# Optimization experiments

Measured on AMD Instinct MI355X. Metric: run time of the kernel, lower is better.

The kernel has to match this reference:

```python
import jax, jax.numpy as jnp
import numpy as np

N, D = 8192, 256
ALPHA, BETA, K = 50.0, 1.0, 2


def setup_inputs() -> dict:
    key = jax.random.key(0)
    k1, k2, k3, k4 = jax.random.split(key, 4)
    Q = jax.random.normal(k1, (N, D), dtype=jnp.float32)
    # 0/1 similarity structure; diagonal forced nonzero so no row is fully masked
    sim = jax.random.randint(k2, (N, N), 0, 2).astype(jnp.float32)
    sim = sim.at[jnp.arange(N), jnp.arange(N)].set(1.0)
    # nn.Linear(in_dim, in_dim) params: y = x @ W.T + b
    bound = 1.0 / np.sqrt(D)
    W = jax.random.uniform(k3, (D, D), jnp.float32, -bound, bound)
    b = jax.random.uniform(k4, (D,), jnp.float32, -bound, bound)
    return {"Q": Q, "sim_mat": sim, "W": W, "b": b}


def reference(Q, sim_mat, W, b):
    mask = sim_mat == 0  # (N, N) bool, constant across iterations
    H = Q
    for _ in range(K):
        H_proj = H @ W.T + b                      # (N, d)
        scores = H_proj @ H_proj.T                # (N, N)
        scores = jnp.where(mask, -jnp.inf, scores)
        lamb = jax.nn.softmax(scores, axis=1)     # (N, N)
        numerator = ALPHA * Q + BETA * (lamb @ H)
        denominator = ALPHA + BETA * jnp.sum(lamb, axis=1, keepdims=True)
        H = numerator / denominator
    return H
```

## Files before the change

### kernel.cpp

```cpp
#include <hip/hip_runtime.h>
#include <hip/hip_bf16.h>

#define NN 8192
#define DD 256
#define ALPHA 50.0f
#define BETA 1.0f
#define THR 10.0f
#define KQ 8
#define KEYS (NN / KQ)
#define STEPS (KEYS / 32)
#define QROWS 128

typedef __attribute__((ext_vector_type(8))) short short8;
typedef __attribute__((ext_vector_type(4))) float f32x4;

static __device__ __forceinline__ ushort f2bf(float f) {
    union { __hip_bfloat16 h; ushort u; } v;
    v.h = __float2bfloat16(f);
    return v.u;
}
static __device__ __forceinline__ float bf2f(ushort u) {
    union { unsigned u; float f; } v; v.u = ((unsigned)u) << 16;
    return v.f;
}
static __device__ __forceinline__ void gl_lds16(const void* g, void* l) {
    __builtin_amdgcn_global_load_lds(
        (const __attribute__((address_space(1))) unsigned int*)g,
        (__attribute__((address_space(3))) unsigned int*)l, 16, 0, 0);
}

__global__ void k_wconv(const float* __restrict__ W, ushort* __restrict__ Wb) {
    int i = blockIdx.x * 256 + threadIdx.x;
    Wb[i] = f2bf(W[i]);
}

__global__ __launch_bounds__(256) void k_pack(const float* __restrict__ sim,
                                              unsigned* __restrict__ bits) {
    __shared__ unsigned char nibs[256];
    int row = blockIdx.x;
    int tid = threadIdx.x;
    for (int p = 0; p < 8; ++p) {
        int col = p * 1024 + tid * 4;
        float4 v = *reinterpret_cast<const float4*>(sim + (size_t)row * NN + col);
        unsigned char nib = (unsigned char)((v.x != 0.f) | ((v.y != 0.f) << 1) |
                                            ((v.z != 0.f) << 2) | ((v.w != 0.f) << 3));
        nibs[tid] = nib;
        __syncthreads();
        if (tid < 32) {
            unsigned word = 0;
#pragma unroll
            for (int i = 0; i < 8; ++i) word |= ((unsigned)nibs[tid * 8 + i]) << (4 * i);
            bits[row * (NN / 32) + p * 32 + tid] = word;
        }
        __syncthreads();
    }
}

__global__ __launch_bounds__(256) void k_convert(const float* __restrict__ H,
                                                 ushort* __restrict__ Hv,
                                                 ushort* __restrict__ Hvt) {
    __shared__ ushort T[64][72];
    int tile = blockIdx.x;
    int r0 = (tile >> 2) * 64;
    int c0 = (tile & 3) * 64;
    int tid = threadIdx.x;
    int tr = tid >> 4;
    int tc = (tid & 15) * 4;
    for (int i = 0; i < 4; ++i) {
        int r = tr + i * 16;
        float4 v = *reinterpret_cast<const float4*>(H + (size_t)(r0 + r) * DD + c0 + tc);
        ushort4 o;
        o.x = f2bf(v.x); o.y = f2bf(v.y); o.z = f2bf(v.z); o.w = f2bf(v.w);
        *reinterpret_cast<ushort4*>(Hv + (size_t)(r0 + r) * DD + c0 + tc) = o;
        T[tc + 0][r] = o.x; T[tc + 1][r] = o.y; T[tc + 2][r] = o.z; T[tc + 3][r] = o.w;
    }
    __syncthreads();
    for (int i = 0; i < 4; ++i) {
        int c = tr + i * 16;
        ushort4 o;
        o.x = T[c][tc + 0]; o.y = T[c][tc + 1]; o.z = T[c][tc + 2]; o.w = T[c][tc + 3];
        *reinterpret_cast<ushort4*>(Hvt + (size_t)(c0 + c) * NN + r0 + tc) = o;
    }
}

__global__ __launch_bounds__(256) void k_proj(const ushort* __restrict__ Hv,
                                              const ushort* __restrict__ Wb,
                                              const float* __restrict__ b,
                                              ushort* __restrict__ Hp) {
    int w = threadIdx.x >> 6;
    int lane = threadIdx.x & 63;
    int row0 = (blockIdx.x >> 1) * 64 + w * 16;
    int ch = blockIdx.x & 1;
    int lr = lane & 15;
    int lk = lane >> 4;
    short8 af[8];
    for (int kk = 0; kk < 8; ++kk)
        af[kk] = *reinterpret_cast<const short8*>(Hv + (size_t)(row0 + lr) * DD + kk * 32 + lk * 8);
    for (int t = 0; t < 8; ++t) {
        f32x4 acc = {0.f, 0.f, 0.f, 0.f};
        int col = (ch * 8 + t) * 16 + lr;
        for (int kk = 0; kk < 8; ++kk) {
            short8 bf = *reinterpret_cast<const short8*>(Wb + (size_t)col * DD + kk * 32 + lk * 8);
            acc = __builtin_amdgcn_mfma_f32_16x16x32_bf16(af[kk], bf, acc, 0, 0, 0);
        }
        float bias = b[col];
        for (int j = 0; j < 4; ++j) {
            int row = row0 + lk * 4 + j;
            Hp[(size_t)row * DD + col] = f2bf(acc[j] + bias);
        }
    }
}

#define PSTR 40
#define KBYTES (32 * 256 * 2)
#define VBYTES (256 * 32 * 2)
#define PBYTES (8 * 16 * PSTR * 2)
#define BBYTES (QROWS * 32 * 4)
#define SMEM_ATTN (3 * KBYTES + 3 * VBYTES + PBYTES + BBYTES)
__global__ __launch_bounds__(512) void k_attn(const ushort* __restrict__ Hp,
                                              const ushort* __restrict__ Hvt,
                                              const unsigned* __restrict__ bits,
                                              ushort* __restrict__ Opart,
                                              float* __restrict__ mpart,
                                              float* __restrict__ lpart) {
    extern __shared__ char smem[];
    ushort* KlB = (ushort*)smem;
    ushort* VlB = (ushort*)(smem + 3 * KBYTES);
    ushort* Pl  = (ushort*)(smem + 3 * KBYTES + 3 * VBYTES);
    unsigned* Bl = (unsigned*)(smem + 3 * KBYTES + 3 * VBYTES + PBYTES);

    const int tid = threadIdx.x;
    const int w = tid >> 6;
    const int lane = tid & 63;
    const int lr = lane & 15;
    const int lk = lane >> 4;
    const int bid = blockIdx.x;
    const int kq = bid & 7;
    const int qt = bid >> 3;
    const int rw0 = qt * QROWS + w * 16;
    const int kstart = kq * KEYS;

    int kSrc[2], vSrc[2], dstO[2];
#pragma unroll
    for (int i = 0; i < 2; ++i) {
        int S = i * 512 + tid;
        int rK = S >> 5, cpK = S & 31;
        kSrc[i] = rK * 256 + (cpK ^ (rK & 7)) * 8;
        int rV = S >> 2, cpV = S & 3;
        vSrc[i] = rV * NN + (cpV ^ ((rV >> 2) & 3)) * 8;
        dstO[i] = S * 8;
    }
    auto stageK = [&](int buf, int kb) {
        const ushort* Kg = Hp + (size_t)kb * DD;
        ushort* base = KlB + buf * (32 * 256);
#pragma unroll
        for (int i = 0; i < 2; ++i) gl_lds16(Kg + kSrc[i], base + dstO[i]);
    };
    auto stageV = [&](int buf, int kb) {
        const ushort* Vg = Hvt + kb;
        ushort* base = VlB + buf * (256 * 32);
#pragma unroll
        for (int i = 0; i < 2; ++i) gl_lds16(Vg + vSrc[i], base + dstO[i]);
    };

    int Koff[8];
#pragma unroll
    for (int kk = 0; kk < 8; ++kk)
        Koff[kk] = (lr << 9) + ((((kk << 2) + lk) ^ (lr & 7)) << 4);
    const int vBase = (lr << 6) + ((lk ^ ((lr >> 2) & 3)) << 4);

    short8 qf[8];
#pragma unroll
    for (int kk = 0; kk < 8; ++kk)
        qf[kk] = *reinterpret_cast<const short8*>(Hp + (size_t)(rw0 + lr) * DD + kk * 32 + lk * 8);

    f32x4 o[17];
#pragma unroll
    for (int t = 0; t < 17; ++t) o[t] = {0.f, 0.f, 0.f, 0.f};
    float m[4] = {-1e30f, -1e30f, -1e30f, -1e30f};

    short8 ones;
#pragma unroll
    for (int e = 0; e < 8; ++e) ones[e] = (short)0x3f80;

    {
        const unsigned* Bg = bits + (size_t)(qt * QROWS) * (NN / 32) + kq * 32;
#pragma unroll
        for (int i = 0; i < 2; ++i) {
            int S = i * 512 + tid;
            int r = S >> 3, c = S & 7;
            gl_lds16(Bg + (size_t)r * (NN / 32) + c * 4, Bl + S * 4);
        }
    }
    stageK(0, kstart);
    stageV(0, kstart);
    stageK(1, kstart + 32);
    stageV(1, kstart + 32);
    asm volatile("s_waitcnt vmcnt(4)" ::: "memory");
    __builtin_amdgcn_s_barrier();
    __builtin_amdgcn_sched_barrier(0);

    ushort* Pw = Pl + (size_t)w * 16 * PSTR;
    const int mrow = (w * 16 + lk * 4) * 32;
    int cur = 0;
    for (int step = 0; step < STEPS; ++step) {
        const int kb = kstart + step * 32;
        const bool staged = (step + 2 < STEPS);
        if (staged) {
            int nb = cur + 2; if (nb >= 3) nb -= 3;
            stageK(nb, kb + 64);
            stageV(nb, kb + 64);
        }
        unsigned mwj[4];
#pragma unroll
        for (int j = 0; j < 4; ++j) mwj[j] = Bl[mrow + j * 32 + step];

        const char* Kb = (const char*)(KlB + cur * (32 * 256));
        f32x4 s0 = {0.f, 0.f, 0.f, 0.f}, s1 = {0.f, 0.f, 0.f, 0.f};
        __builtin_amdgcn_s_setprio(1);
#pragma unroll
        for (int kk = 0; kk < 8; ++kk) {
            short8 k0 = *reinterpret_cast<const short8*>(Kb + Koff[kk]);
            short8 k1 = *reinterpret_cast<const short8*>(Kb + Koff[kk] + (16 << 9));
            s0 = __builtin_amdgcn_mfma_f32_16x16x32_bf16(qf[kk], k0, s0, 0, 0, 0);
            s1 = __builtin_amdgcn_mfma_f32_16x16x32_bf16(qf[kk], k1, s1, 0, 0, 0);
        }
        __builtin_amdgcn_s_setprio(0);
        float c = -1e30f;
#pragma unroll
        for (int j = 0; j < 4; ++j) {
            float a0 = ((mwj[j] >> lr) & 1u) ? s0[j] : -1e30f;
            float a1 = ((mwj[j] >> (lr + 16)) & 1u) ? s1[j] : -1e30f;
            s0[j] = a0; s1[j] = a1;
            c = fmaxf(c, fmaxf(a0, a1) - m[j]);
        }
        if (__any(c > THR)) {
#pragma unroll
            for (int j = 0; j < 4; ++j) {
                float mx = fmaxf(s0[j], s1[j]);
                mx = fmaxf(mx, __shfl_xor(mx, 1));
                mx = fmaxf(mx, __shfl_xor(mx, 2));
                mx = fmaxf(mx, __shfl_xor(mx, 4));
                mx = fmaxf(mx, __shfl_xor(mx, 8));
                float mn = fmaxf(m[j], mx);
                float scale = __expf(m[j] - mn);
                m[j] = mn;
#pragma unroll
                for (int t = 0; t < 17; ++t) o[t][j] *= scale;
            }
        }
#pragma unroll
        for (int j = 0; j < 4; ++j) {
            Pw[(lk * 4 + j) * PSTR + lr]      = f2bf(__expf(s0[j] - m[j]));
            Pw[(lk * 4 + j) * PSTR + 16 + lr] = f2bf(__expf(s1[j] - m[j]));
        }
        asm volatile("s_waitcnt lgkmcnt(0)" ::: "memory");
        __builtin_amdgcn_sched_barrier(0);
        short8 pa = *reinterpret_cast<const short8*>(Pw + lr * PSTR + lk * 8);
        const char* Vb = (const char*)(VlB + cur * (256 * 32));
        __builtin_amdgcn_s_setprio(1);
#pragma unroll
        for (int t = 0; t < 16; ++t) {
            short8 vf = *reinterpret_cast<const short8*>(Vb + vBase + (t << 10));
            o[t] = __builtin_amdgcn_mfma_f32_16x16x32_bf16(pa, vf, o[t], 0, 0, 0);
        }
        o[16] = __builtin_amdgcn_mfma_f32_16x16x32_bf16(pa, ones, o[16], 0, 0, 0);
        __builtin_amdgcn_s_setprio(0);
        if (staged) asm volatile("s_waitcnt vmcnt(4)" ::: "memory");
        else        asm volatile("s_waitcnt vmcnt(0)" ::: "memory");
        __builtin_amdgcn_s_barrier();
        __builtin_amdgcn_sched_barrier(0);
        cur = (cur == 2) ? 0 : cur + 1;
    }

    ushort* op = Opart + ((size_t)kq * NN + rw0) * DD;
#pragma unroll
    for (int t = 0; t < 16; ++t)
#pragma unroll
        for (int j = 0; j < 4; ++j)
            op[(size_t)(lk * 4 + j) * DD + t * 16 + lr] = f2bf(o[t][j]);
    if (lr == 0) {
#pragma unroll
        for (int j = 0; j < 4; ++j) {
            mpart[kq * NN + rw0 + lk * 4 + j] = m[j];
            lpart[kq * NN + rw0 + lk * 4 + j] = o[16][j];
        }
    }
}

__global__ __launch_bounds__(256) void k_merge8(const ushort* __restrict__ Opart,
                                                const float* __restrict__ mpart,
                                                const float* __restrict__ lpart,
                                                const float* __restrict__ Qo,
                                                float* __restrict__ dst) {
    int w = threadIdx.x >> 6;
    int lane = threadIdx.x & 63;
    int r0 = blockIdx.x * 32 + w * 8;
    for (int rr = 0; rr < 8; ++rr) {
        int r = r0 + rr;
        float mv[8], f[8];
        float M = -1e30f;
#pragma unroll
        for (int p = 0; p < 8; ++p) { mv[p] = mpart[p * NN + r]; M = fmaxf(M, mv[p]); }
        float L = 0.f;
#pragma unroll
        for (int p = 0; p < 8; ++p) { f[p] = __expf(mv[p] - M); L += f[p] * lpart[p * NN + r]; }
        float invL = 1.0f / L;
        int c = lane * 4;
        float a0 = 0.f, a1 = 0.f, a2 = 0.f, a3 = 0.f;
#pragma unroll
        for (int p = 0; p < 8; ++p) {
            ushort4 u = *reinterpret_cast<const ushort4*>(Opart + ((size_t)p * NN + r) * DD + c);
            a0 += f[p] * bf2f(u.x); a1 += f[p] * bf2f(u.y);
            a2 += f[p] * bf2f(u.z); a3 += f[p] * bf2f(u.w);
        }
        float4 qv = *reinterpret_cast<const float4*>(Qo + (size_t)r * DD + c);
        float4 ov;
        ov.x = (ALPHA * qv.x + a0 * invL) * (1.0f / (ALPHA + BETA));
        ov.y = (ALPHA * qv.y + a1 * invL) * (1.0f / (ALPHA + BETA));
        ov.z = (ALPHA * qv.z + a2 * invL) * (1.0f / (ALPHA + BETA));
        ov.w = (ALPHA * qv.w + a3 * invL) * (1.0f / (ALPHA + BETA));
        *reinterpret_cast<float4*>(dst + (size_t)r * DD + c) = ov;
    }
}

extern "C" void kernel_launch(void* const* d_in, const int* in_sizes, int n_in,
                              void* d_out, int out_size, void* d_ws, size_t ws_size,
                              hipStream_t stream) {
    const float* Q   = (const float*)d_in[0];
    const float* sim = (const float*)d_in[1];
    const float* W   = (const float*)d_in[2];
    const float* b   = (const float*)d_in[3];
    float* out = (float*)d_out;

    char* ws = (char*)d_ws;
    size_t off = 0;
    ushort* Hv   = (ushort*)(ws + off); off += (size_t)NN * DD * 2;
    ushort* HvtA = (ushort*)(ws + off); off += (size_t)NN * DD * 2;
    ushort* HvtB = (ushort*)(ws + off); off += (size_t)NN * DD * 2;
    ushort* Hp   = (ushort*)(ws + off); off += (size_t)NN * DD * 2;
    ushort* Wb   = (ushort*)(ws + off); off += (size_t)DD * DD * 2;
    unsigned* bits = (unsigned*)(ws + off); off += (size_t)NN * (NN / 32) * 4;
    float*  H1   = (float*)(ws + off);  off += (size_t)NN * DD * 4;
    ushort* Opart = (ushort*)(ws + off); off += (size_t)KQ * NN * DD * 2;
    float*  mpart = (float*)(ws + off);  off += (size_t)KQ * NN * 4;
    float*  lpart = (float*)(ws + off);  off += (size_t)KQ * NN * 4;

    (void)hipFuncSetAttribute((const void*)k_attn,
                              hipFuncAttributeMaxDynamicSharedMemorySize, SMEM_ATTN);

    k_wconv<<<DD * DD / 256, 256, 0, stream>>>(W, Wb);
    k_pack<<<NN, 256, 0, stream>>>(sim, bits);
    k_convert<<<(NN / 64) * (DD / 64), 256, 0, stream>>>(Q, Hv, HvtA);

    k_proj<<<NN / 32, 256, 0, stream>>>(Hv, Wb, b, Hp);
    k_attn<<<(NN / QROWS) * KQ, 512, SMEM_ATTN, stream>>>(Hp, HvtA, bits, Opart, mpart, lpart);
    k_merge8<<<NN / 32, 256, 0, stream>>>(Opart, mpart, lpart, Q, H1);
    k_convert<<<(NN / 64) * (DD / 64), 256, 0, stream>>>(H1, Hv, HvtB);

    k_proj<<<NN / 32, 256, 0, stream>>>(Hv, Wb, b, Hp);
    k_attn<<<(NN / QROWS) * KQ, 512, SMEM_ATTN, stream>>>(Hp, HvtB, bits, Opart, mpart, lpart);
    k_merge8<<<NN / 32, 256, 0, stream>>>(Opart, mpart, lpart, Q, out);
}
```

Measured before the change: 351.5 us.

## Load K fragments directly into registers instead of staging through LDS

Removes the triple-buffered K tile in shared memory. Each wave now prefetches its own K MFMA fragments from global memory into registers one step ahead, with vmcnt waits adjusted to match. This cuts LDS footprint and LDS reads for the QK^T product. The cost is redundant global loads across the 8 waves and 64 more vector registers per lane, which risks spills or lower occupancy.

```diff
diff --git a/kernel.cpp b/kernel.cpp
--- a/kernel.cpp
+++ b/kernel.cpp
@@ -112,11 +112,10 @@
 }
 
 #define PSTR 40
-#define KBYTES (32 * 256 * 2)
 #define VBYTES (256 * 32 * 2)
 #define PBYTES (8 * 16 * PSTR * 2)
 #define BBYTES (QROWS * 32 * 4)
-#define SMEM_ATTN (3 * KBYTES + 3 * VBYTES + PBYTES + BBYTES)
+#define SMEM_ATTN (3 * VBYTES + PBYTES + BBYTES)
 __global__ __launch_bounds__(512) void k_attn(const ushort* __restrict__ Hp,
                                               const ushort* __restrict__ Hvt,
                                               const unsigned* __restrict__ bits,
@@ -124,10 +123,9 @@
                                               float* __restrict__ mpart,
                                               float* __restrict__ lpart) {
     extern __shared__ char smem[];
-    ushort* KlB = (ushort*)smem;
-    ushort* VlB = (ushort*)(smem + 3 * KBYTES);
-    ushort* Pl  = (ushort*)(smem + 3 * KBYTES + 3 * VBYTES);
-    unsigned* Bl = (unsigned*)(smem + 3 * KBYTES + 3 * VBYTES + PBYTES);
+    ushort* VlB = (ushort*)smem;
+    ushort* Pl  = (ushort*)(smem + 3 * VBYTES);
+    unsigned* Bl = (unsigned*)(smem + 3 * VBYTES + PBYTES);
 
     const int tid = threadIdx.x;
     const int w = tid >> 6;
@@ -140,22 +138,14 @@
     const int rw0 = qt * QROWS + w * 16;
     const int kstart = kq * KEYS;
 
-    int kSrc[2], vSrc[2], dstO[2];
+    int vSrc[2], dstO[2];
 #pragma unroll
     for (int i = 0; i < 2; ++i) {
         int S = i * 512 + tid;
-        int rK = S >> 5, cpK = S & 31;
-        kSrc[i] = rK * 256 + (cpK ^ (rK & 7)) * 8;
         int rV = S >> 2, cpV = S & 3;
         vSrc[i] = rV * NN + (cpV ^ ((rV >> 2) & 3)) * 8;
         dstO[i] = S * 8;
     }
-    auto stageK = [&](int buf, int kb) {
-        const ushort* Kg = Hp + (size_t)kb * DD;
-        ushort* base = KlB + buf * (32 * 256);
-#pragma unroll
-        for (int i = 0; i < 2; ++i) gl_lds16(Kg + kSrc[i], base + dstO[i]);
-    };
     auto stageV = [&](int buf, int kb) {
         const ushort* Vg = Hvt + kb;
         ushort* base = VlB + buf * (256 * 32);
@@ -163,10 +153,6 @@
         for (int i = 0; i < 2; ++i) gl_lds16(Vg + vSrc[i], base + dstO[i]);
     };
 
-    int Koff[8];
-#pragma unroll
-    for (int kk = 0; kk < 8; ++kk)
-        Koff[kk] = (lr << 9) + ((((kk << 2) + lk) ^ (lr & 7)) << 4);
     const int vBase = (lr << 6) + ((lk ^ ((lr >> 2) & 3)) << 4);
 
     short8 qf[8];
@@ -192,11 +178,19 @@
             gl_lds16(Bg + (size_t)r * (NN / 32) + c * 4, Bl + S * 4);
         }
     }
-    stageK(0, kstart);
     stageV(0, kstart);
-    stageK(1, kstart + 32);
     stageV(1, kstart + 32);
-    asm volatile("s_waitcnt vmcnt(4)" ::: "memory");
+    short8 kreg[16];
+    {
+        const ushort* kp0 = Hp + (size_t)(kstart + lr) * DD + lk * 8;
+        const ushort* kp1 = kp0 + (size_t)16 * DD;
+#pragma unroll
+        for (int kk = 0; kk < 8; ++kk) {
+            kreg[kk]     = *reinterpret_cast<const short8*>(kp0 + kk * 32);
+            kreg[8 + kk] = *reinterpret_cast<const short8*>(kp1 + kk * 32);
+        }
+    }
+    asm volatile("s_waitcnt vmcnt(18)" ::: "memory");
     __builtin_amdgcn_s_barrier();
     __builtin_amdgcn_sched_barrier(0);
 
@@ -205,27 +199,31 @@
     int cur = 0;
     for (int step = 0; step < STEPS; ++step) {
         const int kb = kstart + step * 32;
-        const bool staged = (step + 2 < STEPS);
-        if (staged) {
+        if (step + 2 < STEPS) {
             int nb = cur + 2; if (nb >= 3) nb -= 3;
-            stageK(nb, kb + 64);
             stageV(nb, kb + 64);
         }
         unsigned mwj[4];
 #pragma unroll
         for (int j = 0; j < 4; ++j) mwj[j] = Bl[mrow + j * 32 + step];
 
-        const char* Kb = (const char*)(KlB + cur * (32 * 256));
         f32x4 s0 = {0.f, 0.f, 0.f, 0.f}, s1 = {0.f, 0.f, 0.f, 0.f};
         __builtin_amdgcn_s_setprio(1);
 #pragma unroll
         for (int kk = 0; kk < 8; ++kk) {
-            short8 k0 = *reinterpret_cast<const short8*>(Kb + Koff[kk]);
-            short8 k1 = *reinterpret_cast<const short8*>(Kb + Koff[kk] + (16 << 9));
-            s0 = __builtin_amdgcn_mfma_f32_16x16x32_bf16(qf[kk], k0, s0, 0, 0, 0);
-            s1 = __builtin_amdgcn_mfma_f32_16x16x32_bf16(qf[kk], k1, s1, 0, 0, 0);
+            s0 = __builtin_amdgcn_mfma_f32_16x16x32_bf16(qf[kk], kreg[kk], s0, 0, 0, 0);
+            s1 = __builtin_amdgcn_mfma_f32_16x16x32_bf16(qf[kk], kreg[8 + kk], s1, 0, 0, 0);
         }
         __builtin_amdgcn_s_setprio(0);
+        if (step + 1 < STEPS) {
+            const ushort* kp0 = Hp + (size_t)(kb + 32 + lr) * DD + lk * 8;
+            const ushort* kp1 = kp0 + (size_t)16 * DD;
+#pragma unroll
+            for (int kk = 0; kk < 8; ++kk) {
+                kreg[kk]     = *reinterpret_cast<const short8*>(kp0 + kk * 32);
+                kreg[8 + kk] = *reinterpret_cast<const short8*>(kp1 + kk * 32);
+            }
+        }
         float c = -1e30f;
 #pragma unroll
         for (int j = 0; j < 4; ++j) {
@@ -266,10 +264,15 @@
         }
         o[16] = __builtin_amdgcn_mfma_f32_16x16x32_bf16(pa, ones, o[16], 0, 0, 0);
         __builtin_amdgcn_s_setprio(0);
-        if (staged) asm volatile("s_waitcnt vmcnt(4)" ::: "memory");
-        else        asm volatile("s_waitcnt vmcnt(0)" ::: "memory");
-        __builtin_amdgcn_s_barrier();
-        __builtin_amdgcn_sched_barrier(0);
+        if (step + 2 < STEPS) {
+            asm volatile("s_waitcnt vmcnt(18)" ::: "memory");
+            __builtin_amdgcn_s_barrier();
+            __builtin_amdgcn_sched_barrier(0);
+        } else if (step + 1 < STEPS) {
+            asm volatile("s_waitcnt vmcnt(16)" ::: "memory");
+            __builtin_amdgcn_s_barrier();
+            __builtin_amdgcn_sched_barrier(0);
+        }
         cur = (cur == 2) ? 0 : cur + 1;
     }
 
```

After: 616.6 us. +75.5%, slower.

## Use 64-key tiles with double buffering and one barrier per tile in attention

Applied to the files above, without the earlier changes.

The attention kernel now processes 64 keys per iteration instead of 32. It moves from a triple-buffered 32-key pipeline to a double-buffered 64-key pipeline, which halves the number of block barriers and keeps LDS use about the same. The V tile layout and its swizzle change to match the 64-key width. The QK MFMAs for both 32-key halves are issued together before the two softmax and PV halves run. The cost is a shallower prefetch (one tile ahead with a full vmcnt(0) wait) and higher register pressure from four score accumulators.

```diff
diff --git a/kernel.cpp b/kernel.cpp
--- a/kernel.cpp
+++ b/kernel.cpp
@@ -8,7 +8,8 @@
 #define THR 10.0f
 #define KQ 8
 #define KEYS (NN / KQ)
-#define STEPS (KEYS / 32)
+#define KTILE 64
+#define ITERS (KEYS / KTILE)
 #define QROWS 128
 
 typedef __attribute__((ext_vector_type(8))) short short8;
@@ -112,11 +113,11 @@
 }
 
 #define PSTR 40
-#define KBYTES (32 * 256 * 2)
-#define VBYTES (256 * 32 * 2)
+#define KBYTES (KTILE * 256 * 2)
+#define VBYTES (256 * KTILE * 2)
 #define PBYTES (8 * 16 * PSTR * 2)
 #define BBYTES (QROWS * 32 * 4)
-#define SMEM_ATTN (3 * KBYTES + 3 * VBYTES + PBYTES + BBYTES)
+#define SMEM_ATTN (2 * KBYTES + 2 * VBYTES + PBYTES + BBYTES)
 __global__ __launch_bounds__(512) void k_attn(const ushort* __restrict__ Hp,
                                               const ushort* __restrict__ Hvt,
                                               const unsigned* __restrict__ bits,
@@ -125,9 +126,9 @@
                                               float* __restrict__ lpart) {
     extern __shared__ char smem[];
     ushort* KlB = (ushort*)smem;
-    ushort* VlB = (ushort*)(smem + 3 * KBYTES);
-    ushort* Pl  = (ushort*)(smem + 3 * KBYTES + 3 * VBYTES);
-    unsigned* Bl = (unsigned*)(smem + 3 * KBYTES + 3 * VBYTES + PBYTES);
+    ushort* VlB = (ushort*)(smem + 2 * KBYTES);
+    ushort* Pl  = (ushort*)(smem + 2 * KBYTES + 2 * VBYTES);
+    unsigned* Bl = (unsigned*)(smem + 2 * KBYTES + 2 * VBYTES + PBYTES);
 
     const int tid = threadIdx.x;
     const int w = tid >> 6;
@@ -140,34 +141,35 @@
     const int rw0 = qt * QROWS + w * 16;
     const int kstart = kq * KEYS;
 
-    int kSrc[2], vSrc[2], dstO[2];
-#pragma unroll
-    for (int i = 0; i < 2; ++i) {
+    int kSrc[4], vSrc[4], dstO[4];
+#pragma unroll
+    for (int i = 0; i < 4; ++i) {
         int S = i * 512 + tid;
         int rK = S >> 5, cpK = S & 31;
         kSrc[i] = rK * 256 + (cpK ^ (rK & 7)) * 8;
-        int rV = S >> 2, cpV = S & 3;
-        vSrc[i] = rV * NN + (cpV ^ ((rV >> 2) & 3)) * 8;
+        int rV = S >> 3, cpV = S & 7;
+        vSrc[i] = rV * NN + (cpV ^ (rV & 7)) * 8;
         dstO[i] = S * 8;
     }
     auto stageK = [&](int buf, int kb) {
         const ushort* Kg = Hp + (size_t)kb * DD;
-        ushort* base = KlB + buf * (32 * 256);
-#pragma unroll
-        for (int i = 0; i < 2; ++i) gl_lds16(Kg + kSrc[i], base + dstO[i]);
+        ushort* base = KlB + buf * (KTILE * 256);
+#pragma unroll
+        for (int i = 0; i < 4; ++i) gl_lds16(Kg + kSrc[i], base + dstO[i]);
     };
     auto stageV = [&](int buf, int kb) {
         const ushort* Vg = Hvt + kb;
-        ushort* base = VlB + buf * (256 * 32);
-#pragma unroll
-        for (int i = 0; i < 2; ++i) gl_lds16(Vg + vSrc[i], base + dstO[i]);
+        ushort* base = VlB + buf * (256 * KTILE);
+#pragma unroll
+        for (int i = 0; i < 4; ++i) gl_lds16(Vg + vSrc[i], base + dstO[i]);
     };
 
     int Koff[8];
 #pragma unroll
     for (int kk = 0; kk < 8; ++kk)
         Koff[kk] = (lr << 9) + ((((kk << 2) + lk) ^ (lr & 7)) << 4);
-    const int vBase = (lr << 6) + ((lk ^ ((lr >> 2) & 3)) << 4);
+    const int vBaseA = (lr << 7) + ((lk ^ (lr & 7)) << 4);
+    const int vBaseB = (lr << 7) + (((4 + lk) ^ (lr & 7)) << 4);
 
     short8 qf[8];
 #pragma unroll
@@ -194,83 +196,133 @@
     }
     stageK(0, kstart);
     stageV(0, kstart);
-    stageK(1, kstart + 32);
-    stageV(1, kstart + 32);
-    asm volatile("s_waitcnt vmcnt(4)" ::: "memory");
+    asm volatile("s_waitcnt vmcnt(0)" ::: "memory");
     __builtin_amdgcn_s_barrier();
     __builtin_amdgcn_sched_barrier(0);
 
     ushort* Pw = Pl + (size_t)w * 16 * PSTR;
     const int mrow = (w * 16 + lk * 4) * 32;
     int cur = 0;
-    for (int step = 0; step < STEPS; ++step) {
-        const int kb = kstart + step * 32;
-        const bool staged = (step + 2 < STEPS);
+    for (int it = 0; it < ITERS; ++it) {
+        const int kb = kstart + it * KTILE;
+        const bool staged = (it + 1 < ITERS);
         if (staged) {
-            int nb = cur + 2; if (nb >= 3) nb -= 3;
-            stageK(nb, kb + 64);
-            stageV(nb, kb + 64);
-        }
-        unsigned mwj[4];
-#pragma unroll
-        for (int j = 0; j < 4; ++j) mwj[j] = Bl[mrow + j * 32 + step];
-
-        const char* Kb = (const char*)(KlB + cur * (32 * 256));
-        f32x4 s0 = {0.f, 0.f, 0.f, 0.f}, s1 = {0.f, 0.f, 0.f, 0.f};
+            stageK(cur ^ 1, kb + KTILE);
+            stageV(cur ^ 1, kb + KTILE);
+        }
+        unsigned mwa[4], mwb[4];
+#pragma unroll
+        for (int j = 0; j < 4; ++j) {
+            mwa[j] = Bl[mrow + j * 32 + it * 2];
+            mwb[j] = Bl[mrow + j * 32 + it * 2 + 1];
+        }
+
+        const char* Kb = (const char*)(KlB + cur * (KTILE * 256));
+        f32x4 s0a = {0.f,0.f,0.f,0.f}, s1a = {0.f,0.f,0.f,0.f};
+        f32x4 s0b = {0.f,0.f,0.f,0.f}, s1b = {0.f,0.f,0.f,0.f};
         __builtin_amdgcn_s_setprio(1);
 #pragma unroll
         for (int kk = 0; kk < 8; ++kk) {
-            short8 k0 = *reinterpret_cast<const short8*>(Kb + Koff[kk]);
-            short8 k1 = *reinterpret_cast<const short8*>(Kb + Koff[kk] + (16 << 9));
-            s0 = __builtin_amdgcn_mfma_f32_16x16x32_bf16(qf[kk], k0, s0, 0, 0, 0);
-            s1 = __builtin_amdgcn_mfma_f32_16x16x32_bf16(qf[kk], k1, s1, 0, 0, 0);
+            short8 k0a = *reinterpret_cast<const short8*>(Kb + Koff[kk]);
+            short8 k1a = *reinterpret_cast<const short8*>(Kb + Koff[kk] + (16 << 9));
+            short8 k0b = *reinterpret_cast<const short8*>(Kb + Koff[kk] + (32 << 9));
+            short8 k1b = *reinterpret_cast<const short8*>(Kb + Koff[kk] + (48 << 9));
+            s0a = __builtin_amdgcn_mfma_f32_16x16x32_bf16(qf[kk], k0a, s0a, 0, 0, 0);
+            s1a = __builtin_amdgcn_mfma_f32_16x16x32_bf16(qf[kk], k1a, s1a, 0, 0, 0);
+            s0b = __builtin_amdgcn_mfma_f32_16x16x32_bf16(qf[kk], k0b, s0b, 0, 0, 0);
+            s1b = __builtin_amdgcn_mfma_f32_16x16x32_bf16(qf[kk], k1b, s1b, 0, 0, 0);
         }
         __builtin_amdgcn_s_setprio(0);
-        float c = -1e30f;
-#pragma unroll
-        for (int j = 0; j < 4; ++j) {
-            float a0 = ((mwj[j] >> lr) & 1u) ? s0[j] : -1e30f;
-            float a1 = ((mwj[j] >> (lr + 16)) & 1u) ? s1[j] : -1e30f;
-            s0[j] = a0; s1[j] = a1;
-            c = fmaxf(c, fmaxf(a0, a1) - m[j]);
-        }
-        if (__any(c > THR)) {
+
+        const char* Vb = (const char*)(VlB + cur * (256 * KTILE));
+        {
+            float c = -1e30f;
 #pragma unroll
             for (int j = 0; j < 4; ++j) {
-                float mx = fmaxf(s0[j], s1[j]);
-                mx = fmaxf(mx, __shfl_xor(mx, 1));
-                mx = fmaxf(mx, __shfl_xor(mx, 2));
-                mx = fmaxf(mx, __shfl_xor(mx, 4));
-                mx = fmaxf(mx, __shfl_xor(mx, 8));
-                float mn = fmaxf(m[j], mx);
-                float scale = __expf(m[j] - mn);
-                m[j] = mn;
-#pragma unroll
-                for (int t = 0; t < 17; ++t) o[t][j] *= scale;
-            }
-        }
-#pragma unroll
-        for (int j = 0; j < 4; ++j) {
-            Pw[(lk * 4 + j) * PSTR + lr]      = f2bf(__expf(s0[j] - m[j]));
-            Pw[(lk * 4 + j) * PSTR + 16 + lr] = f2bf(__expf(s1[j] - m[j]));
-        }
-        asm volatile("s_waitcnt lgkmcnt(0)" ::: "memory");
-        __builtin_amdgcn_sched_barrier(0);
-        short8 pa = *reinterpret_cast<const short8*>(Pw + lr * PSTR + lk * 8);
-        const char* Vb = (const char*)(VlB + cur * (256 * 32));
-        __builtin_amdgcn_s_setprio(1);
-#pragma unroll
-        for (int t = 0; t < 16; ++t) {
-            short8 vf = *reinterpret_cast<const short8*>(Vb + vBase + (t << 10));
-            o[t] = __builtin_amdgcn_mfma_f32_16x16x32_bf16(pa, vf, o[t], 0, 0, 0);
-        }
-        o[16] = __builtin_amdgcn_mfma_f32_16x16x32_bf16(pa, ones, o[16], 0, 0, 0);
-        __builtin_amdgcn_s_setprio(0);
-        if (staged) asm volatile("s_waitcnt vmcnt(4)" ::: "memory");
-        else        asm volatile("s_waitcnt vmcnt(0)" ::: "memory");
-        __builtin_amdgcn_s_barrier();
-        __builtin_amdgcn_sched_barrier(0);
-        cur = (cur == 2) ? 0 : cur + 1;
+                float a0 = ((mwa[j] >> lr) & 1u) ? s0a[j] : -1e30f;
+                float a1 = ((mwa[j] >> (lr + 16)) & 1u) ? s1a[j] : -1e30f;
+                s0a[j] = a0; s1a[j] = a1;
+                c = fmaxf(c, fmaxf(a0, a1) - m[j]);
+            }
+            if (__any(c > THR)) {
+#pragma unroll
+                for (int j = 0; j < 4; ++j) {
+                    float mx = fmaxf(s0a[j], s1a[j]);
+                    mx = fmaxf(mx, __shfl_xor(mx, 1));
+                    mx = fmaxf(mx, __shfl_xor(mx, 2));
+                    mx = fmaxf(mx, __shfl_xor(mx, 4));
+                    mx = fmaxf(mx, __shfl_xor(mx, 8));
+                    float mn = fmaxf(m[j], mx);
+                    float scale = __expf(m[j] - mn);
+                    m[j] = mn;
+#pragma unroll
+                    for (int t = 0; t < 17; ++t) o[t][j] *= scale;
+                }
+            }
+#pragma unroll
+            for (int j = 0; j < 4; ++j) {
+                Pw[(lk * 4 + j) * PSTR + lr]      = f2bf(__expf(s0a[j] - m[j]));
+                Pw[(lk * 4 + j) * PSTR + 16 + lr] = f2bf(__expf(s1a[j] - m[j]));
+            }
+            asm volatile("s_waitcnt lgkmcnt(0)" ::: "memory");
+            __builtin_amdgcn_sched_barrier(0);
+            short8 pa = *reinterpret_cast<const short8*>(Pw + lr * PSTR + lk * 8);
+            __builtin_amdgcn_s_setprio(1);
+#pragma unroll
+            for (int t = 0; t < 16; ++t) {
+                short8 vf = *reinterpret_cast<const short8*>(Vb + vBaseA + (t << 11));
+                o[t] = __builtin_amdgcn_mfma_f32_16x16x32_bf16(pa, vf, o[t], 0, 0, 0);
+            }
+            o[16] = __builtin_amdgcn_mfma_f32_16x16x32_bf16(pa, ones, o[16], 0, 0, 0);
+            __builtin_amdgcn_s_setprio(0);
+        }
+        {
+            float c = -1e30f;
+#pragma unroll
+            for (int j = 0; j < 4; ++j) {
+                float a0 = ((mwb[j] >> lr) & 1u) ? s0b[j] : -1e30f;
+                float a1 = ((mwb[j] >> (lr + 16)) & 1u) ? s1b[j] : -1e30f;
+                s0b[j] = a0; s1b[j] = a1;
+                c = fmaxf(c, fmaxf(a0, a1) - m[j]);
+            }
+            if (__any(c > THR)) {
+#pragma unroll
+                for (int j = 0; j < 4; ++j) {
+                    float mx = fmaxf(s0b[j], s1b[j]);
+                    mx = fmaxf(mx, __shfl_xor(mx, 1));
+                    mx = fmaxf(mx, __shfl_xor(mx, 2));
+                    mx = fmaxf(mx, __shfl_xor(mx, 4));
+                    mx = fmaxf(mx, __shfl_xor(mx, 8));
+                    float mn = fmaxf(m[j], mx);
+                    float scale = __expf(m[j] - mn);
+                    m[j] = mn;
+#pragma unroll
+                    for (int t = 0; t < 17; ++t) o[t][j] *= scale;
+                }
+            }
+#pragma unroll
+            for (int j = 0; j < 4; ++j) {
+                Pw[(lk * 4 + j) * PSTR + lr]      = f2bf(__expf(s0b[j] - m[j]));
+                Pw[(lk * 4 + j) * PSTR + 16 + lr] = f2bf(__expf(s1b[j] - m[j]));
+            }
+            asm volatile("s_waitcnt lgkmcnt(0)" ::: "memory");
+            __builtin_amdgcn_sched_barrier(0);
+            short8 pb = *reinterpret_cast<const short8*>(Pw + lr * PSTR + lk * 8);
+            __builtin_amdgcn_s_setprio(1);
+#pragma unroll
+            for (int t = 0; t < 16; ++t) {
+                short8 vf = *reinterpret_cast<const short8*>(Vb + vBaseB + (t << 11));
+                o[t] = __builtin_amdgcn_mfma_f32_16x16x32_bf16(pb, vf, o[t], 0, 0, 0);
+            }
+            o[16] = __builtin_amdgcn_mfma_f32_16x16x32_bf16(pb, ones, o[16], 0, 0, 0);
+            __builtin_amdgcn_s_setprio(0);
+        }
+        if (staged) {
+            asm volatile("s_waitcnt vmcnt(0)" ::: "memory");
+            __builtin_amdgcn_s_barrier();
+            __builtin_amdgcn_sched_barrier(0);
+        }
+        cur ^= 1;
     }
 
     ushort* op = Opart + ((size_t)kq * NN + rw0) * DD;
```

Result: faster. 330.5 us, median of 2 (-6.0%).
